# Kernel tuning notes

Measured on AMD Instinct MI355X. Metric: run time of the kernel, lower is better.

## Reference

```python
import jax, jax.numpy as jnp
import numpy as np

R = 8
EPS = 1e-08
EPSS = 1e-12


def _diff_x(x, r):
    left = x[:, :, r:2 * r + 1]
    middle = x[:, :, 2 * r + 1:] - x[:, :, :-2 * r - 1]
    right = x[:, :, -1:] - x[:, :, -2 * r - 1:-r - 1]
    return jnp.concatenate([left, middle, right], axis=2)


def _diff_y(x, r):
    left = x[:, :, :, r:2 * r + 1]
    middle = x[:, :, :, 2 * r + 1:] - x[:, :, :, :-2 * r - 1]
    right = x[:, :, :, -1:] - x[:, :, :, -2 * r - 1:-r - 1]
    return jnp.concatenate([left, middle, right], axis=3)


def box_filter(x, r):
    # cumsum-based (2r+1)x(2r+1) box sum with clamped borders (matches torch BoxFilter)
    return _diff_y(jnp.cumsum(_diff_x(jnp.cumsum(x, axis=2), r), axis=3), r)


def bilinear_resize(x, H, W):
    # F.interpolate(mode='bilinear', align_corners=True) for NCHW
    n, c, h, w = x.shape
    ys = jnp.linspace(0.0, h - 1.0, H)
    xs = jnp.linspace(0.0, w - 1.0, W)
    y0 = jnp.floor(ys).astype(jnp.int32)
    x0 = jnp.floor(xs).astype(jnp.int32)
    y1 = jnp.minimum(y0 + 1, h - 1)
    x1 = jnp.minimum(x0 + 1, w - 1)
    wy = (ys - y0).astype(x.dtype)[None, None, :, None]
    wx = (xs - x0).astype(x.dtype)[None, None, None, :]
    rows = jnp.take(x, y0, axis=2) * (1.0 - wy) + jnp.take(x, y1, axis=2) * wy
    return jnp.take(rows, x0, axis=3) * (1.0 - wx) + jnp.take(rows, x1, axis=3) * wx


def setup_inputs() -> dict:
    key = jax.random.key(0)
    k1, k2, k3, k4 = jax.random.split(key, 4)
    return {
        "lr_x": jax.random.normal(k1, (4, 3, 256, 256), dtype=jnp.float32),
        "lr_y": jax.random.normal(k2, (4, 3, 256, 256), dtype=jnp.float32),
        "hr_x": jax.random.normal(k3, (4, 3, 1024, 1024), dtype=jnp.float32),
        "l_a": jax.random.uniform(k4, (4, 3, 256, 256), dtype=jnp.float32),
    }


def reference(lr_x, lr_y, hr_x, l_a):
    n, c, h, w = lr_x.shape
    _, _, hh, wh = hr_x.shape
    dt = lr_x.dtype

    N = box_filter(jnp.ones((1, 1, h, w), dtype=dt), R)  # local window counts

    l_a = jnp.abs(l_a) + EPSS
    l_t = l_a / jnp.sum(l_a)

    mean_a = box_filter(l_a) if False else box_filter(l_a, R) / N
    mean_a2xy = box_filter(l_a * l_a * lr_x * lr_y, R) / N
    mean_tax = box_filter(l_t * l_a * lr_x, R) / N
    mean_ay = box_filter(l_a * lr_y, R) / N
    mean_a2x2 = box_filter(l_a * l_a * lr_x * lr_x, R) / N
    mean_ax = box_filter(l_a * lr_x, R) / N

    temp = jnp.abs(mean_a2x2 - N * mean_tax * mean_ax)
    A = (mean_a2xy - N * mean_tax * mean_ay) / (temp + EPS)
    b = (mean_ay - A * mean_ax) / mean_a

    A = box_filter(A, R) / N
    b = box_filter(b, R) / N

    mean_A = bilinear_resize(A, hh, wh)
    mean_b = bilinear_resize(b, hh, wh)
    return (mean_A * hr_x + mean_b).astype(jnp.float32)
```

## Files before the change

kernel.cpp:

```cpp
#include <hip/hip_runtime.h>

#define RAD 8
#define HH 256
#define WW 256
#define NC 12
#define PS (HH*WW)

__device__ __forceinline__ int swz(int b) { return (b & 7) * 96 + (b >> 3); }

__global__ __launch_bounds__(256) void k_hbox6(const float* __restrict__ la,
                                               const float* __restrict__ lx,
                                               const float* __restrict__ ly,
                                               float* __restrict__ Hbuf,
                                               float* __restrict__ partials) {
    int c  = swz(blockIdx.x);
    int p  = c >> 6;
    int rc = c & 63;
    int base = p * PS + rc * 4 * WW;
    int tid = threadIdx.x, lane = tid & 63, wid = tid >> 6;
    __shared__ float wtot[6][4];
    __shared__ float Pref[6][WW];
    __shared__ float ls[4];
    float asum = 0.0f;
    int  j1    = min(tid + RAD, WW - 1);
    bool hasj0 = (tid - RAD) > 0;
    int  j0m1  = tid - RAD - 1;
    for (int rr = 0; rr < 4; rr++) {
        int o = base + rr * WW + tid;
        float a  = fabsf(la[o]) + 1e-12f;
        float xv = lx[o];
        float yv = ly[o];
        asum += a;
        float ax = a * xv, ay = a * yv;
        float v0 = a, v1 = ax, v2 = ay, v3 = a * ax, v4 = ax * ax, v5 = ax * ay;
        #pragma unroll
        for (int off = 1; off < 64; off <<= 1) {
            float t0 = __shfl_up(v0, off, 64), t1 = __shfl_up(v1, off, 64),
                  t2 = __shfl_up(v2, off, 64), t3 = __shfl_up(v3, off, 64),
                  t4 = __shfl_up(v4, off, 64), t5 = __shfl_up(v5, off, 64);
            if (lane >= off) { v0 += t0; v1 += t1; v2 += t2; v3 += t3; v4 += t4; v5 += t5; }
        }
        if (lane == 63) {
            wtot[0][wid] = v0; wtot[1][wid] = v1; wtot[2][wid] = v2;
            wtot[3][wid] = v3; wtot[4][wid] = v4; wtot[5][wid] = v5;
        }
        __syncthreads();
        float a0 = 0, a1 = 0, a2 = 0, a3 = 0, a4 = 0, a5 = 0;
        for (int w = 0; w < wid; w++) {
            a0 += wtot[0][w]; a1 += wtot[1][w]; a2 += wtot[2][w];
            a3 += wtot[3][w]; a4 += wtot[4][w]; a5 += wtot[5][w];
        }
        Pref[0][tid] = v0 + a0; Pref[1][tid] = v1 + a1; Pref[2][tid] = v2 + a2;
        Pref[3][tid] = v3 + a3; Pref[4][tid] = v4 + a4; Pref[5][tid] = v5 + a5;
        __syncthreads();
        #pragma unroll
        for (int k = 0; k < 6; k++) {
            float s = Pref[k][j1] - (hasj0 ? Pref[k][j0m1] : 0.0f);
            Hbuf[k * NC * PS + o] = s;
        }
    }
    for (int off = 32; off > 0; off >>= 1) asum += __shfl_down(asum, off, 64);
    if (lane == 0) ls[wid] = asum;
    __syncthreads();
    if (tid == 0) partials[blockIdx.x] = ls[0] + ls[1] + ls[2] + ls[3];
}

__global__ __launch_bounds__(256) void k_vab(const float* __restrict__ Hbuf,
                                             const float* __restrict__ partials,
                                             float* __restrict__ HA,
                                             float* __restrict__ HB) {
    int c  = swz(blockIdx.x);
    int p  = c >> 6;
    int i0 = (c & 63) * 4;
    int tid = threadIdx.x, lane = tid & 63, wid = tid >> 6;
    __shared__ float wtot[2][4];
    __shared__ float Pref[2][WW];
    __shared__ float ls[4];
    __shared__ float sS;

    float psum = partials[tid] + partials[tid + 256] + partials[tid + 512];
    for (int off = 32; off > 0; off >>= 1) psum += __shfl_down(psum, off, 64);
    if (lane == 0) ls[wid] = psum;
    __syncthreads();
    if (tid == 0) sS = ls[0] + ls[1] + ls[2] + ls[3];
    __syncthreads();
    float invS = 1.0f / sS;

    const float* Hp = Hbuf + p * PS + tid;
    float s0 = 0, s1 = 0, s2 = 0, s3 = 0, s4 = 0, s5 = 0;
    int lo = max(i0 - RAD, 0), hi = min(i0 + RAD, HH - 1);
    for (int i = lo; i <= hi; i++) {
        int o = i * WW;
        s0 += Hp[0 * NC * PS + o]; s1 += Hp[1 * NC * PS + o]; s2 += Hp[2 * NC * PS + o];
        s3 += Hp[3 * NC * PS + o]; s4 += Hp[4 * NC * PS + o]; s5 += Hp[5 * NC * PS + o];
    }
    float cx = (float)(min(tid + RAD, WW - 1) - max(tid - RAD, 0) + 1);
    int  j1c   = min(tid + RAD, WW - 1);
    bool hasj0 = (tid - RAD) > 0;
    int  j0m1  = tid - RAD - 1;
    for (int i = i0; i < i0 + 4; i++) {
        if (i > i0) {
            int add = i + RAD, sub = i - RAD - 1;
            if (add <= HH - 1) {
                int o = add * WW;
                s0 += Hp[0 * NC * PS + o]; s1 += Hp[1 * NC * PS + o]; s2 += Hp[2 * NC * PS + o];
                s3 += Hp[3 * NC * PS + o]; s4 += Hp[4 * NC * PS + o]; s5 += Hp[5 * NC * PS + o];
            }
            if (sub >= 0) {
                int o = sub * WW;
                s0 -= Hp[0 * NC * PS + o]; s1 -= Hp[1 * NC * PS + o]; s2 -= Hp[2 * NC * PS + o];
                s3 -= Hp[3 * NC * PS + o]; s4 -= Hp[4 * NC * PS + o]; s5 -= Hp[5 * NC * PS + o];
            }
        }
        float cy = (float)(min(i + RAD, HH - 1) - max(i - RAD, 0) + 1);
        float Nv = cx * cy;
        float invN = 1.0f / Nv;
        float mean_a    = s0 * invN;
        float mean_ax   = s1 * invN;
        float mean_ay   = s2 * invN;
        float mean_tax  = s3 * invN * invS;
        float mean_a2x2 = s4 * invN;
        float mean_a2xy = s5 * invN;
        float temp = fabsf(mean_a2x2 - Nv * mean_tax * mean_ax);
        float Av = (mean_a2xy - Nv * mean_tax * mean_ay) / (temp + 1e-8f);
        float bv = (mean_ay - Av * mean_ax) / mean_a;

        float v0 = Av, v1 = bv;
        #pragma unroll
        for (int off = 1; off < 64; off <<= 1) {
            float t0 = __shfl_up(v0, off, 64), t1 = __shfl_up(v1, off, 64);
            if (lane >= off) { v0 += t0; v1 += t1; }
        }
        if (lane == 63) { wtot[0][wid] = v0; wtot[1][wid] = v1; }
        __syncthreads();
        float a0 = 0, a1 = 0;
        for (int w = 0; w < wid; w++) { a0 += wtot[0][w]; a1 += wtot[1][w]; }
        Pref[0][tid] = v0 + a0; Pref[1][tid] = v1 + a1;
        __syncthreads();
        int o = p * PS + i * WW + tid;
        HA[o] = Pref[0][j1c] - (hasj0 ? Pref[0][j0m1] : 0.0f);
        HB[o] = Pref[1][j1c] - (hasj0 ? Pref[1][j0m1] : 0.0f);
    }
}

__global__ __launch_bounds__(256) void k_vbox2(const float* __restrict__ HA,
                                               const float* __restrict__ HB,
                                               float* __restrict__ mA,
                                               float* __restrict__ mB) {
    int c  = swz(blockIdx.x);
    int p  = c >> 6;
    int i0 = (c & 63) * 4;
    int col = threadIdx.x;
    const float* a = HA + p * PS + col;
    const float* b = HB + p * PS + col;
    float sa = 0, sb = 0;
    int lo = max(i0 - RAD, 0), hi = min(i0 + RAD, HH - 1);
    for (int i = lo; i <= hi; i++) { sa += a[i * WW]; sb += b[i * WW]; }
    float cx = (float)(min(col + RAD, WW - 1) - max(col - RAD, 0) + 1);
    for (int i = i0; i < i0 + 4; i++) {
        if (i > i0) {
            if (i + RAD <= HH - 1) { sa += a[(i + RAD) * WW]; sb += b[(i + RAD) * WW]; }
            if (i - RAD - 1 >= 0)  { sa -= a[(i - RAD - 1) * WW]; sb -= b[(i - RAD - 1) * WW]; }
        }
        float cy = (float)(min(i + RAD, HH - 1) - max(i - RAD, 0) + 1);
        float inv = 1.0f / (cx * cy);
        mA[p * PS + i * WW + col] = sa * inv;
        mB[p * PS + i * WW + col] = sb * inv;
    }
}

__global__ __launch_bounds__(256) void k_resize(const float* __restrict__ mA,
                                                const float* __restrict__ mB,
                                                const float* __restrict__ hrx,
                                                float* __restrict__ out) {
    int idx = blockIdx.x * 256 + threadIdx.x;
    int p   = idx >> 18;
    int rem = idx & ((1 << 18) - 1);
    int I   = rem >> 8;
    int J4  = (rem & 255) << 2;
    const float scale = 255.0f / 1023.0f;
    float ysf = (float)I * scale;
    int   y0  = (int)ysf;
    float wy  = ysf - (float)y0;
    int   y1  = min(y0 + 1, HH - 1);
    const float* a0p = mA + p * PS + y0 * WW;
    const float* a1p = mA + p * PS + y1 * WW;
    const float* b0p = mB + p * PS + y0 * WW;
    const float* b1p = mB + p * PS + y1 * WW;
    int xb = (int)((float)J4 * scale);
    int i1 = min(xb + 1, WW - 1);
    int i2 = min(xb + 2, WW - 1);
    float A0a = a0p[xb], A0b = a0p[i1], A0c = a0p[i2];
    float A1a = a1p[xb], A1b = a1p[i1], A1c = a1p[i2];
    float B0a = b0p[xb], B0b = b0p[i1], B0c = b0p[i2];
    float B1a = b1p[xb], B1b = b1p[i1], B1c = b1p[i2];
    float4 h = ((const float4*)hrx)[idx];
    float hv[4] = {h.x, h.y, h.z, h.w};
    float ov[4];
    float omwy = 1.0f - wy;
    #pragma unroll
    for (int k = 0; k < 4; k++) {
        float xsk = (float)(J4 + k) * scale;
        int   x0  = (int)xsk;
        float wx  = xsk - (float)x0;
        bool hisel = (x0 > xb);
        float Alo0 = hisel ? A0b : A0a, Ahi0 = hisel ? A0c : A0b;
        float Alo1 = hisel ? A1b : A1a, Ahi1 = hisel ? A1c : A1b;
        float Blo0 = hisel ? B0b : B0a, Bhi0 = hisel ? B0c : B0b;
        float Blo1 = hisel ? B1b : B1a, Bhi1 = hisel ? B1c : B1b;
        float omwx = 1.0f - wx;
        float Ar0 = Alo0 * omwx + Ahi0 * wx;
        float Ar1 = Alo1 * omwx + Ahi1 * wx;
        float Br0 = Blo0 * omwx + Bhi0 * wx;
        float Br1 = Blo1 * omwx + Bhi1 * wx;
        float Avv = Ar0 * omwy + Ar1 * wy;
        float Bvv = Br0 * omwy + Br1 * wy;
        ov[k] = Avv * hv[k] + Bvv;
    }
    float4 o;
    o.x = ov[0]; o.y = ov[1]; o.z = ov[2]; o.w = ov[3];
    ((float4*)out)[idx] = o;
}

extern "C" void kernel_launch(void* const* d_in, const int* in_sizes, int n_in,
                              void* d_out, int out_size, void* d_ws, size_t ws_size,
                              hipStream_t stream) {
    const float* lr_x = (const float*)d_in[0];
    const float* lr_y = (const float*)d_in[1];
    const float* hr_x = (const float*)d_in[2];
    const float* l_a  = (const float*)d_in[3];
    float* out = (float*)d_out;

    float* ws       = (float*)d_ws;
    float* partials = ws;
    float* Hbuf     = ws + 1024;
    float* HA       = Hbuf + 6 * NC * PS;
    float* HB       = HA + NC * PS;
    float* mA       = HB + NC * PS;
    float* mB       = mA + NC * PS;

    k_hbox6 <<<NC * 64, 256, 0, stream>>>(l_a, lr_x, lr_y, Hbuf, partials);
    k_vab   <<<NC * 64, 256, 0, stream>>>(Hbuf, partials, HA, HB);
    k_vbox2 <<<NC * 64, 256, 0, stream>>>(HA, HB, mA, mB);
    k_resize<<<(NC * 1024 * 1024 / 4) / 256, 256, 0, stream>>>(mA, mB, hr_x, out);
}
```

Measured before the change: 151.1 us.

## Fuse box filters, coefficient solve and resize into one tiled kernel

Replaces the four-kernel pipeline with a small global-sum kernel plus a single fused kernel. Each block loads a haloed low-res tile into shared memory, computes both box-filter passes and the A/b solve in LDS with sliding-window sums, then writes its 128x128 high-res output tile directly. This removes the large global intermediate buffers (six H planes, HA/HB, mA/mB) and their round trips. In exchange, halo rows and columns are recomputed across tiles. The large shared-memory footprint also limits the kernel to one 512-thread block per CU, with low thread utilisation in the box-filter stages.

```diff
diff --git a/kernel.cpp b/kernel.cpp
--- a/kernel.cpp
+++ b/kernel.cpp
@@ -5,221 +5,262 @@
 #define WW 256
 #define NC 12
 #define PS (HH*WW)
+#define SCALE (255.0f/1023.0f)
+
+#define NREG 68
+#define NMID 52
+#define NCEN 36
+#define INP  69
+#define HP   53
+#define CP   37
+#define HS   (NREG*HP)
 
 __device__ __forceinline__ int swz(int b) { return (b & 7) * 96 + (b >> 3); }
 
-__global__ __launch_bounds__(256) void k_hbox6(const float* __restrict__ la,
-                                               const float* __restrict__ lx,
-                                               const float* __restrict__ ly,
-                                               float* __restrict__ Hbuf,
-                                               float* __restrict__ partials) {
-    int c  = swz(blockIdx.x);
-    int p  = c >> 6;
-    int rc = c & 63;
-    int base = p * PS + rc * 4 * WW;
-    int tid = threadIdx.x, lane = tid & 63, wid = tid >> 6;
-    __shared__ float wtot[6][4];
-    __shared__ float Pref[6][WW];
+__global__ __launch_bounds__(256) void k_reduce(const float* __restrict__ la,
+                                                float* __restrict__ partials) {
+    int tid = threadIdx.x;
     __shared__ float ls[4];
-    float asum = 0.0f;
-    int  j1    = min(tid + RAD, WW - 1);
-    bool hasj0 = (tid - RAD) > 0;
-    int  j0m1  = tid - RAD - 1;
-    for (int rr = 0; rr < 4; rr++) {
-        int o = base + rr * WW + tid;
-        float a  = fabsf(la[o]) + 1e-12f;
-        float xv = lx[o];
-        float yv = ly[o];
-        asum += a;
-        float ax = a * xv, ay = a * yv;
-        float v0 = a, v1 = ax, v2 = ay, v3 = a * ax, v4 = ax * ax, v5 = ax * ay;
-        #pragma unroll
-        for (int off = 1; off < 64; off <<= 1) {
-            float t0 = __shfl_up(v0, off, 64), t1 = __shfl_up(v1, off, 64),
-                  t2 = __shfl_up(v2, off, 64), t3 = __shfl_up(v3, off, 64),
-                  t4 = __shfl_up(v4, off, 64), t5 = __shfl_up(v5, off, 64);
-            if (lane >= off) { v0 += t0; v1 += t1; v2 += t2; v3 += t3; v4 += t4; v5 += t5; }
-        }
-        if (lane == 63) {
-            wtot[0][wid] = v0; wtot[1][wid] = v1; wtot[2][wid] = v2;
-            wtot[3][wid] = v3; wtot[4][wid] = v4; wtot[5][wid] = v5;
-        }
-        __syncthreads();
-        float a0 = 0, a1 = 0, a2 = 0, a3 = 0, a4 = 0, a5 = 0;
-        for (int w = 0; w < wid; w++) {
-            a0 += wtot[0][w]; a1 += wtot[1][w]; a2 += wtot[2][w];
-            a3 += wtot[3][w]; a4 += wtot[4][w]; a5 += wtot[5][w];
-        }
-        Pref[0][tid] = v0 + a0; Pref[1][tid] = v1 + a1; Pref[2][tid] = v2 + a2;
-        Pref[3][tid] = v3 + a3; Pref[4][tid] = v4 + a4; Pref[5][tid] = v5 + a5;
-        __syncthreads();
-        #pragma unroll
-        for (int k = 0; k < 6; k++) {
-            float s = Pref[k][j1] - (hasj0 ? Pref[k][j0m1] : 0.0f);
-            Hbuf[k * NC * PS + o] = s;
-        }
-    }
-    for (int off = 32; off > 0; off >>= 1) asum += __shfl_down(asum, off, 64);
-    if (lane == 0) ls[wid] = asum;
+    const float4* p4 = (const float4*)la;
+    int base = blockIdx.x * 2048 + tid;
+    float s = 0.f;
+    #pragma unroll
+    for (int i = 0; i < 8; i++) {
+        float4 v = p4[base + i * 256];
+        s += (fabsf(v.x) + 1e-12f) + (fabsf(v.y) + 1e-12f) +
+             (fabsf(v.z) + 1e-12f) + (fabsf(v.w) + 1e-12f);
+    }
+    for (int off = 32; off > 0; off >>= 1) s += __shfl_down(s, off, 64);
+    int lane = tid & 63, wid = tid >> 6;
+    if (lane == 0) ls[wid] = s;
     __syncthreads();
     if (tid == 0) partials[blockIdx.x] = ls[0] + ls[1] + ls[2] + ls[3];
 }
 
-__global__ __launch_bounds__(256) void k_vab(const float* __restrict__ Hbuf,
-                                             const float* __restrict__ partials,
-                                             float* __restrict__ HA,
-                                             float* __restrict__ HB) {
-    int c  = swz(blockIdx.x);
-    int p  = c >> 6;
-    int i0 = (c & 63) * 4;
-    int tid = threadIdx.x, lane = tid & 63, wid = tid >> 6;
-    __shared__ float wtot[2][4];
-    __shared__ float Pref[2][WW];
-    __shared__ float ls[4];
-    __shared__ float sS;
-
-    float psum = partials[tid] + partials[tid + 256] + partials[tid + 512];
-    for (int off = 32; off > 0; off >>= 1) psum += __shfl_down(psum, off, 64);
-    if (lane == 0) ls[wid] = psum;
-    __syncthreads();
-    if (tid == 0) sS = ls[0] + ls[1] + ls[2] + ls[3];
-    __syncthreads();
-    float invS = 1.0f / sS;
-
-    const float* Hp = Hbuf + p * PS + tid;
-    float s0 = 0, s1 = 0, s2 = 0, s3 = 0, s4 = 0, s5 = 0;
-    int lo = max(i0 - RAD, 0), hi = min(i0 + RAD, HH - 1);
-    for (int i = lo; i <= hi; i++) {
-        int o = i * WW;
-        s0 += Hp[0 * NC * PS + o]; s1 += Hp[1 * NC * PS + o]; s2 += Hp[2 * NC * PS + o];
-        s3 += Hp[3 * NC * PS + o]; s4 += Hp[4 * NC * PS + o]; s5 += Hp[5 * NC * PS + o];
-    }
-    float cx = (float)(min(tid + RAD, WW - 1) - max(tid - RAD, 0) + 1);
-    int  j1c   = min(tid + RAD, WW - 1);
-    bool hasj0 = (tid - RAD) > 0;
-    int  j0m1  = tid - RAD - 1;
-    for (int i = i0; i < i0 + 4; i++) {
-        if (i > i0) {
-            int add = i + RAD, sub = i - RAD - 1;
-            if (add <= HH - 1) {
-                int o = add * WW;
-                s0 += Hp[0 * NC * PS + o]; s1 += Hp[1 * NC * PS + o]; s2 += Hp[2 * NC * PS + o];
-                s3 += Hp[3 * NC * PS + o]; s4 += Hp[4 * NC * PS + o]; s5 += Hp[5 * NC * PS + o];
+__global__ __launch_bounds__(512, 1) void k_fused(const float* __restrict__ la,
+                                                  const float* __restrict__ lx,
+                                                  const float* __restrict__ ly,
+                                                  const float* __restrict__ hrx,
+                                                  const float* __restrict__ partials,
+                                                  float* __restrict__ out) {
+    __shared__ float sIn[3 * NREG * INP];
+    __shared__ float sH[6 * HS];
+    __shared__ float sred[8];
+    float* inA  = sIn;
+    float* inX  = sIn + NREG * INP;
+    float* inY  = sIn + 2 * NREG * INP;
+    float* Abuf = inA;
+    float* Bbuf = inX;
+    float* HAb  = inY;
+    float* HBb  = inY + NMID * CP;
+    float* mAb  = sH;
+    float* mBb  = sH + NCEN * CP;
+
+    int tid = threadIdx.x;
+    int b  = swz(blockIdx.x);
+    int p  = b >> 6;
+    int t  = b & 63;
+    int ti = t >> 3, tj = t & 7;
+    int I0 = ti << 7, J0 = tj << 7;
+    int Lr0 = max(0, (I0 * 255) / 1023 - 1);
+    int Lc0 = max(0, (J0 * 255) / 1023 - 1);
+
+    {
+        float x = (tid < 96) ? partials[tid] : 0.f;
+        for (int off = 32; off > 0; off >>= 1) x += __shfl_down(x, off, 64);
+        if ((tid & 63) == 0) sred[tid >> 6] = x;
+    }
+
+    int r0g = Lr0 - 16, c0g = Lc0 - 16;
+    const int plane = p * PS;
+    for (unsigned idx = tid; idx < (unsigned)(NREG * NREG); idx += 512u) {
+        int r = (int)(idx / 68u), c = (int)(idx % 68u);
+        int gr = r0g + r, gc = c0g + c;
+        float va = 0.f, vx = 0.f, vy = 0.f;
+        if (gr >= 0 && gr < HH && gc >= 0 && gc < WW) {
+            int off = plane + gr * WW + gc;
+            va = fabsf(la[off]) + 1e-12f;
+            vx = lx[off];
+            vy = ly[off];
+        }
+        int w = r * INP + c;
+        inA[w] = va; inX[w] = vx; inY[w] = vy;
+    }
+    __syncthreads();
+    float invS = 1.0f / (sred[0] + sred[1] + sred[2] + sred[3] +
+                         sred[4] + sred[5] + sred[6] + sred[7]);
+
+    for (unsigned job = tid; job < 272u; job += 512u) {
+        int r = (int)(job % 68u), strip = (int)(job / 68u);
+        const float* rA = inA + r * INP;
+        const float* rX = inX + r * INP;
+        const float* rY = inY + r * INP;
+        float* w0 = sH + r * HP;
+        int c0 = strip * 13;
+        float s0 = 0, s1 = 0, s2 = 0, s3 = 0, s4 = 0, s5 = 0;
+        #pragma unroll
+        for (int c = 0; c < 17; c++) {
+            float a = rA[c0 + c], x = rX[c0 + c], y = rY[c0 + c];
+            float ax = a * x, ay = a * y;
+            s0 += a; s1 += ax; s2 += ay; s3 += a * ax; s4 += ax * ax; s5 += ax * ay;
+        }
+        w0[c0] = s0; w0[HS + c0] = s1; w0[2 * HS + c0] = s2;
+        w0[3 * HS + c0] = s3; w0[4 * HS + c0] = s4; w0[5 * HS + c0] = s5;
+        for (int jm = c0 + 1; jm <= c0 + 12; jm++) {
+            float a = rA[jm + 16], x = rX[jm + 16], y = rY[jm + 16];
+            float ax = a * x, ay = a * y;
+            s0 += a; s1 += ax; s2 += ay; s3 += a * ax; s4 += ax * ax; s5 += ax * ay;
+            a = rA[jm - 1]; x = rX[jm - 1]; y = rY[jm - 1];
+            ax = a * x; ay = a * y;
+            s0 -= a; s1 -= ax; s2 -= ay; s3 -= a * ax; s4 -= ax * ax; s5 -= ax * ay;
+            w0[jm] = s0; w0[HS + jm] = s1; w0[2 * HS + jm] = s2;
+            w0[3 * HS + jm] = s3; w0[4 * HS + jm] = s4; w0[5 * HS + jm] = s5;
+        }
+    }
+    __syncthreads();
+
+    for (unsigned job = tid; job < 208u; job += 512u) {
+        int jm = (int)(job % 52u), strip = (int)(job / 52u);
+        int gjC = Lc0 - 8 + jm;
+        bool cok = (gjC >= 0) && (gjC < WW);
+        float cxw = (float)(min(gjC + RAD, WW - 1) - max(gjC - RAD, 0) + 1);
+        const float* colp = sH + jm;
+        int r0 = strip * 13;
+        float s0 = 0, s1 = 0, s2 = 0, s3 = 0, s4 = 0, s5 = 0;
+        #pragma unroll
+        for (int d = 0; d < 17; d++) {
+            int o = (r0 + d) * HP;
+            s0 += colp[o];          s1 += colp[HS + o];     s2 += colp[2 * HS + o];
+            s3 += colp[3 * HS + o]; s4 += colp[4 * HS + o]; s5 += colp[5 * HS + o];
+        }
+        for (int im = r0; im < r0 + 13; im++) {
+            if (im > r0) {
+                int oa = (im + 16) * HP, os = (im - 1) * HP;
+                s0 += colp[oa] - colp[os];
+                s1 += colp[HS + oa] - colp[HS + os];
+                s2 += colp[2 * HS + oa] - colp[2 * HS + os];
+                s3 += colp[3 * HS + oa] - colp[3 * HS + os];
+                s4 += colp[4 * HS + oa] - colp[4 * HS + os];
+                s5 += colp[5 * HS + oa] - colp[5 * HS + os];
             }
-            if (sub >= 0) {
-                int o = sub * WW;
-                s0 -= Hp[0 * NC * PS + o]; s1 -= Hp[1 * NC * PS + o]; s2 -= Hp[2 * NC * PS + o];
-                s3 -= Hp[3 * NC * PS + o]; s4 -= Hp[4 * NC * PS + o]; s5 -= Hp[5 * NC * PS + o];
+            int giR = Lr0 - 8 + im;
+            float Av = 0.f, bv = 0.f;
+            if (cok && giR >= 0 && giR < HH) {
+                float cyw = (float)(min(giR + RAD, HH - 1) - max(giR - RAD, 0) + 1);
+                float Nv = cxw * cyw, invN = 1.0f / Nv;
+                float m_a = s0 * invN, m_ax = s1 * invN, m_ay = s2 * invN;
+                float m_tax = s3 * invN * invS;
+                float m_a2x2 = s4 * invN, m_a2xy = s5 * invN;
+                float tempv = fabsf(m_a2x2 - Nv * m_tax * m_ax);
+                Av = (m_a2xy - Nv * m_tax * m_ay) / (tempv + 1e-8f);
+                bv = (m_ay - Av * m_ax) / m_a;
             }
-        }
-        float cy = (float)(min(i + RAD, HH - 1) - max(i - RAD, 0) + 1);
-        float Nv = cx * cy;
-        float invN = 1.0f / Nv;
-        float mean_a    = s0 * invN;
-        float mean_ax   = s1 * invN;
-        float mean_ay   = s2 * invN;
-        float mean_tax  = s3 * invN * invS;
-        float mean_a2x2 = s4 * invN;
-        float mean_a2xy = s5 * invN;
-        float temp = fabsf(mean_a2x2 - Nv * mean_tax * mean_ax);
-        float Av = (mean_a2xy - Nv * mean_tax * mean_ay) / (temp + 1e-8f);
-        float bv = (mean_ay - Av * mean_ax) / mean_a;
-
-        float v0 = Av, v1 = bv;
-        #pragma unroll
-        for (int off = 1; off < 64; off <<= 1) {
-            float t0 = __shfl_up(v0, off, 64), t1 = __shfl_up(v1, off, 64);
-            if (lane >= off) { v0 += t0; v1 += t1; }
-        }
-        if (lane == 63) { wtot[0][wid] = v0; wtot[1][wid] = v1; }
-        __syncthreads();
-        float a0 = 0, a1 = 0;
-        for (int w = 0; w < wid; w++) { a0 += wtot[0][w]; a1 += wtot[1][w]; }
-        Pref[0][tid] = v0 + a0; Pref[1][tid] = v1 + a1;
-        __syncthreads();
-        int o = p * PS + i * WW + tid;
-        HA[o] = Pref[0][j1c] - (hasj0 ? Pref[0][j0m1] : 0.0f);
-        HB[o] = Pref[1][j1c] - (hasj0 ? Pref[1][j0m1] : 0.0f);
-    }
-}
-
-__global__ __launch_bounds__(256) void k_vbox2(const float* __restrict__ HA,
-                                               const float* __restrict__ HB,
-                                               float* __restrict__ mA,
-                                               float* __restrict__ mB) {
-    int c  = swz(blockIdx.x);
-    int p  = c >> 6;
-    int i0 = (c & 63) * 4;
-    int col = threadIdx.x;
-    const float* a = HA + p * PS + col;
-    const float* b = HB + p * PS + col;
-    float sa = 0, sb = 0;
-    int lo = max(i0 - RAD, 0), hi = min(i0 + RAD, HH - 1);
-    for (int i = lo; i <= hi; i++) { sa += a[i * WW]; sb += b[i * WW]; }
-    float cx = (float)(min(col + RAD, WW - 1) - max(col - RAD, 0) + 1);
-    for (int i = i0; i < i0 + 4; i++) {
-        if (i > i0) {
-            if (i + RAD <= HH - 1) { sa += a[(i + RAD) * WW]; sb += b[(i + RAD) * WW]; }
-            if (i - RAD - 1 >= 0)  { sa -= a[(i - RAD - 1) * WW]; sb -= b[(i - RAD - 1) * WW]; }
-        }
-        float cy = (float)(min(i + RAD, HH - 1) - max(i - RAD, 0) + 1);
-        float inv = 1.0f / (cx * cy);
-        mA[p * PS + i * WW + col] = sa * inv;
-        mB[p * PS + i * WW + col] = sb * inv;
-    }
-}
-
-__global__ __launch_bounds__(256) void k_resize(const float* __restrict__ mA,
-                                                const float* __restrict__ mB,
-                                                const float* __restrict__ hrx,
-                                                float* __restrict__ out) {
-    int idx = blockIdx.x * 256 + threadIdx.x;
-    int p   = idx >> 18;
-    int rem = idx & ((1 << 18) - 1);
-    int I   = rem >> 8;
-    int J4  = (rem & 255) << 2;
-    const float scale = 255.0f / 1023.0f;
-    float ysf = (float)I * scale;
-    int   y0  = (int)ysf;
-    float wy  = ysf - (float)y0;
-    int   y1  = min(y0 + 1, HH - 1);
-    const float* a0p = mA + p * PS + y0 * WW;
-    const float* a1p = mA + p * PS + y1 * WW;
-    const float* b0p = mB + p * PS + y0 * WW;
-    const float* b1p = mB + p * PS + y1 * WW;
-    int xb = (int)((float)J4 * scale);
-    int i1 = min(xb + 1, WW - 1);
-    int i2 = min(xb + 2, WW - 1);
-    float A0a = a0p[xb], A0b = a0p[i1], A0c = a0p[i2];
-    float A1a = a1p[xb], A1b = a1p[i1], A1c = a1p[i2];
-    float B0a = b0p[xb], B0b = b0p[i1], B0c = b0p[i2];
-    float B1a = b1p[xb], B1b = b1p[i1], B1c = b1p[i2];
-    float4 h = ((const float4*)hrx)[idx];
-    float hv[4] = {h.x, h.y, h.z, h.w};
-    float ov[4];
-    float omwy = 1.0f - wy;
-    #pragma unroll
-    for (int k = 0; k < 4; k++) {
-        float xsk = (float)(J4 + k) * scale;
-        int   x0  = (int)xsk;
-        float wx  = xsk - (float)x0;
-        bool hisel = (x0 > xb);
-        float Alo0 = hisel ? A0b : A0a, Ahi0 = hisel ? A0c : A0b;
-        float Alo1 = hisel ? A1b : A1a, Ahi1 = hisel ? A1c : A1b;
-        float Blo0 = hisel ? B0b : B0a, Bhi0 = hisel ? B0c : B0b;
-        float Blo1 = hisel ? B1b : B1a, Bhi1 = hisel ? B1c : B1b;
-        float omwx = 1.0f - wx;
-        float Ar0 = Alo0 * omwx + Ahi0 * wx;
-        float Ar1 = Alo1 * omwx + Ahi1 * wx;
-        float Br0 = Blo0 * omwx + Bhi0 * wx;
-        float Br1 = Blo1 * omwx + Bhi1 * wx;
-        float Avv = Ar0 * omwy + Ar1 * wy;
-        float Bvv = Br0 * omwy + Br1 * wy;
-        ov[k] = Avv * hv[k] + Bvv;
-    }
-    float4 o;
-    o.x = ov[0]; o.y = ov[1]; o.z = ov[2]; o.w = ov[3];
-    ((float4*)out)[idx] = o;
+            Abuf[im * HP + jm] = Av;
+            Bbuf[im * HP + jm] = bv;
+        }
+    }
+    __syncthreads();
+
+    for (unsigned job = tid; job < 208u; job += 512u) {
+        int row   = (int)(job % 52u);
+        int which = (int)((job / 52u) & 1u);
+        int strip = (int)(job / 104u);
+        const float* rp = (which ? Bbuf : Abuf) + row * HP;
+        float* dst = (which ? HBb : HAb) + row * CP;
+        int c0 = strip * 18;
+        float sum = 0.f;
+        #pragma unroll
+        for (int c = 0; c < 17; c++) sum += rp[c0 + c];
+        dst[c0] = sum;
+        for (int jc = c0 + 1; jc < c0 + 18; jc++) {
+            sum += rp[jc + 16] - rp[jc - 1];
+            dst[jc] = sum;
+        }
+    }
+    __syncthreads();
+
+    for (unsigned job = tid; job < 144u; job += 512u) {
+        int colc  = (int)(job % 36u);
+        int which = (int)((job / 36u) & 1u);
+        int strip = (int)(job / 72u);
+        const float* src = which ? HBb : HAb;
+        float* dst = which ? mBb : mAb;
+        int gjC = Lc0 + colc;
+        float cxw = (float)(min(gjC + RAD, WW - 1) - max(gjC - RAD, 0) + 1);
+        int r0 = strip * 18;
+        float sum = 0.f;
+        #pragma unroll
+        for (int d = 0; d < 17; d++) sum += src[(r0 + d) * CP + colc];
+        for (int ic = r0; ic < r0 + 18; ic++) {
+            if (ic > r0) sum += src[(ic + 16) * CP + colc] - src[(ic - 1) * CP + colc];
+            int giR = Lr0 + ic;
+            float cyw = (float)(min(giR + RAD, HH - 1) - max(giR - RAD, 0) + 1);
+            dst[ic * CP + colc] = sum / (cxw * cyw);
+        }
+    }
+    __syncthreads();
+
+    {
+        int col4 = tid & 31;
+        int rb   = tid >> 5;
+        int J4 = (J0 >> 2) + col4;
+        int Jp = J4 << 2;
+        int xb = (int)((float)Jp * SCALE);
+        int i1 = min(xb + 1, WW - 1), i2 = min(xb + 2, WW - 1);
+        int lxb = xb - Lc0, li1 = i1 - Lc0, li2 = i2 - Lc0;
+        float wxv[4]; bool hs[4];
+        #pragma unroll
+        for (int k = 0; k < 4; k++) {
+            float xsk = (float)(Jp + k) * SCALE;
+            int x0 = (int)xsk;
+            wxv[k] = xsk - (float)x0;
+            hs[k] = (x0 > xb);
+        }
+        const float4* h4 = (const float4*)hrx;
+        float4* o4 = (float4*)out;
+        int planeHR = p * 262144;
+        #pragma unroll
+        for (int it = 0; it < 8; it++) {
+            int row = (it << 4) + rb;
+            int I = I0 + row;
+            float ysf = (float)I * SCALE;
+            int y0 = (int)ysf;
+            float wy = ysf - (float)y0;
+            int y1 = min(y0 + 1, HH - 1);
+            int ly0 = y0 - Lr0, ly1 = y1 - Lr0;
+            const float* a0p = mAb + ly0 * CP;
+            const float* a1p = mAb + ly1 * CP;
+            const float* b0p = mBb + ly0 * CP;
+            const float* b1p = mBb + ly1 * CP;
+            float A0a = a0p[lxb], A0b = a0p[li1], A0c = a0p[li2];
+            float A1a = a1p[lxb], A1b = a1p[li1], A1c = a1p[li2];
+            float B0a = b0p[lxb], B0b = b0p[li1], B0c = b0p[li2];
+            float B1a = b1p[lxb], B1b = b1p[li1], B1c = b1p[li2];
+            int hidx = planeHR + I * 256 + J4;
+            float4 h = h4[hidx];
+            float hv[4] = {h.x, h.y, h.z, h.w};
+            float ov[4];
+            float omwy = 1.0f - wy;
+            #pragma unroll
+            for (int k = 0; k < 4; k++) {
+                bool hb = hs[k];
+                float Alo0 = hb ? A0b : A0a, Ahi0 = hb ? A0c : A0b;
+                float Alo1 = hb ? A1b : A1a, Ahi1 = hb ? A1c : A1b;
+                float Blo0 = hb ? B0b : B0a, Bhi0 = hb ? B0c : B0b;
+                float Blo1 = hb ? B1b : B1a, Bhi1 = hb ? B1c : B1b;
+                float wx = wxv[k], omwx = 1.0f - wx;
+                float Ar0 = Alo0 * omwx + Ahi0 * wx;
+                float Ar1 = Alo1 * omwx + Ahi1 * wx;
+                float Br0 = Blo0 * omwx + Bhi0 * wx;
+                float Br1 = Blo1 * omwx + Bhi1 * wx;
+                float Avv = Ar0 * omwy + Ar1 * wy;
+                float Bvv = Br0 * omwy + Br1 * wy;
+                ov[k] = Avv * hv[k] + Bvv;
+            }
+            float4 o; o.x = ov[0]; o.y = ov[1]; o.z = ov[2]; o.w = ov[3];
+            o4[hidx] = o;
+        }
+    }
 }
 
 extern "C" void kernel_launch(void* const* d_in, const int* in_sizes, int n_in,
@@ -229,18 +270,8 @@
     const float* lr_y = (const float*)d_in[1];
     const float* hr_x = (const float*)d_in[2];
     const float* l_a  = (const float*)d_in[3];
-    float* out = (float*)d_out;
-
-    float* ws       = (float*)d_ws;
-    float* partials = ws;
-    float* Hbuf     = ws + 1024;
-    float* HA       = Hbuf + 6 * NC * PS;
-    float* HB       = HA + NC * PS;
-    float* mA       = HB + NC * PS;
-    float* mB       = mA + NC * PS;
-
-    k_hbox6 <<<NC * 64, 256, 0, stream>>>(l_a, lr_x, lr_y, Hbuf, partials);
-    k_vab   <<<NC * 64, 256, 0, stream>>>(Hbuf, partials, HA, HB);
-    k_vbox2 <<<NC * 64, 256, 0, stream>>>(HA, HB, mA, mB);
-    k_resize<<<(NC * 1024 * 1024 / 4) / 256, 256, 0, stream>>>(mA, mB, hr_x, out);
+    float* partials = (float*)d_ws;
+
+    k_reduce<<<96, 256, 0, stream>>>(l_a, partials);
+    k_fused<<<768, 512, 0, stream>>>(l_a, lr_x, lr_y, hr_x, partials, (float*)d_out);
 }
```

After: 155.1 us. 2.6% more time.
